# Performance work log

Measured on AMD Instinct MI355X. Metric: run time of the kernel, lower is better.

## Reference

```python
import jax, jax.numpy as jnp
import numpy as np

B, R, C, H, W, N = 8, 50, 150, 128, 128, 4096
K = 192  # >= ceil(diagonal of 128x128) = 180, padded line-sample budget
LOSS_WEIGHT = 0.1


def setup_inputs() -> dict:
    key = jax.random.key(0)
    ks = jax.random.split(key, 8)
    rafs = jax.random.normal(ks[0], (B, 2 * R, H, W), jnp.float32)
    heatmaps = jax.random.uniform(ks[1], (B, C, H, W), jnp.float32, minval=0.05, maxval=1.0)
    bi = jax.random.randint(ks[2], (N,), 0, B)
    scls = jax.random.randint(ks[3], (N,), 0, C)
    ocls = jax.random.randint(ks[4], (N,), 0, C)
    syx = jax.random.randint(ks[5], (N, 2), 0, H)
    oyx = jax.random.randint(ks[6], (N, 2), 0, W)
    pred = jax.random.randint(ks[7], (N,), 0, R)
    # ensure subj center != obj center so every relation has nonzero norm (valid)
    same = jnp.all(syx == oyx, axis=1)
    oyx = oyx.at[:, 1].set(jnp.where(same, (oyx[:, 1] + 1) % W, oyx[:, 1]))
    rels = jnp.concatenate(
        [bi[:, None], scls[:, None], syx, ocls[:, None], oyx, pred[:, None]], axis=1
    ).astype(jnp.int32)
    return {"rafs": rafs, "heatmaps": heatmaps, "rels": rels}


def _relation_loss(rafs, heatmaps, rels):
    b, _, h, w = rafs.shape
    raf = jnp.clip(rafs, -1.0, 1.0).reshape(b, -1, 2, h, w)  # [B, R, 2, H, W]
    bi, scls, sy, sx, ocls, oy, ox, pred = (rels[:, i] for i in range(8))
    subj_s = heatmaps[bi, scls, sy, sx]  # [N]
    obj_s = heatmaps[bi, ocls, oy, ox]   # [N]
    # relation unit vector in (x, y) order, obj - subj
    dx = (ox - sx).astype(jnp.float32)
    dy = (oy - sy).astype(jnp.float32)
    norms = jnp.sqrt(dx * dx + dy * dy)  # > 0 by construction (all valid)
    ux, uy = dx / norms, dy / norms
    num = jnp.ceil(norms).astype(jnp.int32)  # number of linspace samples per relation
    # linspace from obj -> subj (matches np.linspace(obj, subj, num)) padded to K
    t = jnp.arange(K, dtype=jnp.float32)[None, :] / jnp.maximum(num - 1, 1).astype(jnp.float32)[:, None]
    px = jnp.rint(ox.astype(jnp.float32)[:, None] + t * (sx - ox).astype(jnp.float32)[:, None]).astype(jnp.int32)
    py = jnp.rint(oy.astype(jnp.float32)[:, None] + t * (sy - oy).astype(jnp.float32)[:, None]).astype(jnp.int32)
    in_len = jnp.arange(K)[None, :] < num[:, None]
    # np.unique dedup: rounded points along a monotone segment repeat only consecutively
    dup = jnp.concatenate(
        [jnp.zeros((px.shape[0], 1), bool), (px[:, 1:] == px[:, :-1]) & (py[:, 1:] == py[:, :-1])],
        axis=1,
    )
    valid = in_len & ~dup  # [N, K]
    vals = raf[bi[:, None], pred[:, None], :, py, px]  # [N, K, 2] gather along the line
    dots = vals[..., 0] * ux[:, None] + vals[..., 1] * uy[:, None]  # [N, K]
    cnt = valid.sum(axis=1).astype(jnp.float32)
    integral = jnp.where(valid, dots, 0.0).sum(axis=1) / cnt  # mean over unique line points
    rel_scores = subj_s * obj_s * jnp.clip(integral, 0.0, 1.0)
    # BCE vs target=1: -log(p) (torch clamps log at -100; eps keeps grads finite)
    logp = jnp.log(jnp.maximum(rel_scores, 1e-12))
    return -logp.mean() * LOSS_WEIGHT


def reference(rafs, heatmaps, rels):
    return _relation_loss(rafs, heatmaps, rels)
```

## Files before the change

kernel.cpp:

```cpp
#include <hip/hip_runtime.h>
#include <math.h>

#define KPTS   192
#define RDIM   50
#define HDIM   128
#define WDIM   128
#define NREL   4096
#define CDIM   150
#define LOSS_W 0.1f
#define WPB    4
#define BLK    (WPB * 64)
#define PLANE  (HDIM * WDIM)

__global__ __launch_bounds__(BLK) void relation_partial_kernel(
    const float* __restrict__ rafs,
    const float* __restrict__ heatmaps,
    const int*   __restrict__ rels,
    float* __restrict__ ws)
{
    const int wave = threadIdx.x >> 6;
    const int lane = threadIdx.x & 63;
    const int rel  = blockIdx.x * WPB + wave;

    const int4* r4 = (const int4*)(rels + (size_t)rel * 8);
    const int4 ra = r4[0];
    const int4 rb = r4[1];
    const int bi   = __builtin_amdgcn_readfirstlane(ra.x);
    const int scls = __builtin_amdgcn_readfirstlane(ra.y);
    const int sy   = __builtin_amdgcn_readfirstlane(ra.z);
    const int sx   = __builtin_amdgcn_readfirstlane(ra.w);
    const int ocls = __builtin_amdgcn_readfirstlane(rb.x);
    const int oy   = __builtin_amdgcn_readfirstlane(rb.y);
    const int ox   = __builtin_amdgcn_readfirstlane(rb.z);
    const int pred = __builtin_amdgcn_readfirstlane(rb.w);

    const float subj = heatmaps[(((size_t)bi * CDIM + (size_t)scls) * HDIM + (size_t)sy) * WDIM + (size_t)sx];
    const float obj  = heatmaps[(((size_t)bi * CDIM + (size_t)ocls) * HDIM + (size_t)oy) * WDIM + (size_t)ox];

    const float dx = (float)(ox - sx);
    const float dy = (float)(oy - sy);
    const float norms = sqrtf(dx * dx + dy * dy);
    const float ux = dx / norms;
    const float uy = dy / norms;
    const int   num = (int)ceilf(norms);
    const float denom = (float)((num - 1) > 1 ? (num - 1) : 1);

    const float oxf = (float)ox, oyf = (float)oy;
    const float sxmox = (float)(sx - ox);
    const float symoy = (float)(sy - oy);

    const size_t rafbase =
        ((size_t)bi * (2 * RDIM) + (size_t)(2 * pred)) * (size_t)PLANE;

    int   pxs[3], pys[3];
    float vxs[3], vys[3];

    #pragma unroll
    for (int s = 0; s < 3; ++s) {
        const int k  = lane + 64 * s;
        const int kk = (k < num) ? k : (num - 1);
        const float t  = (float)kk / denom;
        const int   px = (int)rintf(oxf + t * sxmox);
        const int   py = (int)rintf(oyf + t * symoy);
        pxs[s] = px;
        pys[s] = py;
        const size_t off = (size_t)py * WDIM + (size_t)px;
        vxs[s] = rafs[rafbase + off];
        vys[s] = rafs[rafbase + (size_t)PLANE + off];
    }

    float dot  = 0.0f;
    int   vcnt = 0;
    int   px63 = -1, py63 = -1;

    #pragma unroll
    for (int s = 0; s < 3; ++s) {
        int pxp = __shfl_up(pxs[s], 1, 64);
        int pyp = __shfl_up(pys[s], 1, 64);
        if (lane == 0) { pxp = px63; pyp = py63; }
        px63 = __shfl(pxs[s], 63, 64);
        py63 = __shfl(pys[s], 63, 64);

        const int  k   = lane + 64 * s;
        const bool dup = (pxs[s] == pxp) && (pys[s] == pyp);
        if ((k < num) && !dup) {
            float vx = fminf(fmaxf(vxs[s], -1.0f), 1.0f);
            float vy = fminf(fmaxf(vys[s], -1.0f), 1.0f);
            dot  += vx * ux + vy * uy;
            vcnt += 1;
        }
    }

    #pragma unroll
    for (int off = 32; off > 0; off >>= 1) {
        dot  += __shfl_down(dot,  off, 64);
        vcnt += __shfl_down(vcnt, off, 64);
    }

    if (lane == 0) {
        float integral = dot / (float)vcnt;
        integral = fminf(fmaxf(integral, 0.0f), 1.0f);
        const float rs = subj * obj * integral;
        ws[rel] = logf(fmaxf(rs, 1e-12f));
    }
}

__global__ __launch_bounds__(256) void reduce_kernel(
    const float* __restrict__ part,
    float* __restrict__ out)
{
    const int tid = threadIdx.x;
    float acc = 0.0f;
    #pragma unroll
    for (int j = 0; j < NREL / 256; ++j)
        acc += part[tid + j * 256];

    #pragma unroll
    for (int off = 32; off > 0; off >>= 1)
        acc += __shfl_down(acc, off, 64);

    __shared__ float s[4];
    const int wave = tid >> 6;
    const int lane = tid & 63;
    if (lane == 0) s[wave] = acc;
    __syncthreads();
    if (tid == 0) {
        const float total = s[0] + s[1] + s[2] + s[3];
        out[0] = total * (-LOSS_W / (float)NREL);
    }
}

extern "C" void kernel_launch(void* const* d_in, const int* in_sizes, int n_in,
                              void* d_out, int out_size, void* d_ws, size_t ws_size,
                              hipStream_t stream) {
    const float* rafs     = (const float*)d_in[0];
    const float* heatmaps = (const float*)d_in[1];
    const int*   rels     = (const int*)d_in[2];
    float*       out      = (float*)d_out;
    float*       part     = (float*)d_ws;

    relation_partial_kernel<<<NREL / WPB, BLK, 0, stream>>>(rafs, heatmaps, rels, part);
    reduce_kernel<<<1, 256, 0, stream>>>(part, out);
}
```

Baseline: 138.7 us.

## Stage each RAF plane pair in LDS and bucket relations per block

```diff
diff --git a/kernel.cpp b/kernel.cpp
--- a/kernel.cpp
+++ b/kernel.cpp
@@ -3,105 +3,135 @@
 
 #define KPTS   192
 #define RDIM   50
+#define BDIM   8
 #define HDIM   128
 #define WDIM   128
 #define NREL   4096
 #define CDIM   150
 #define LOSS_W 0.1f
 #define WPB    4
-#define BLK    (WPB * 64)
 #define PLANE  (HDIM * WDIM)
+#define NPAIR  (BDIM * RDIM)
+#define LISTSZ 512
 
-__global__ __launch_bounds__(BLK) void relation_partial_kernel(
+__global__ __launch_bounds__(256) void relation_lds_kernel(
     const float* __restrict__ rafs,
     const float* __restrict__ heatmaps,
     const int*   __restrict__ rels,
     float* __restrict__ ws)
 {
-    const int wave = threadIdx.x >> 6;
-    const int lane = threadIdx.x & 63;
-    const int rel  = blockIdx.x * WPB + wave;
+    __shared__ float plane[2 * PLANE];
+    __shared__ int   list[LISTSZ];
+    __shared__ int   lcnt;
 
-    const int4* r4 = (const int4*)(rels + (size_t)rel * 8);
-    const int4 ra = r4[0];
-    const int4 rb = r4[1];
-    const int bi   = __builtin_amdgcn_readfirstlane(ra.x);
-    const int scls = __builtin_amdgcn_readfirstlane(ra.y);
-    const int sy   = __builtin_amdgcn_readfirstlane(ra.z);
-    const int sx   = __builtin_amdgcn_readfirstlane(ra.w);
-    const int ocls = __builtin_amdgcn_readfirstlane(rb.x);
-    const int oy   = __builtin_amdgcn_readfirstlane(rb.y);
-    const int ox   = __builtin_amdgcn_readfirstlane(rb.z);
-    const int pred = __builtin_amdgcn_readfirstlane(rb.w);
+    const int tid  = threadIdx.x;
+    const int bi_b = blockIdx.x / RDIM;
+    const int pr_b = blockIdx.x - bi_b * RDIM;
 
-    const float subj = heatmaps[(((size_t)bi * CDIM + (size_t)scls) * HDIM + (size_t)sy) * WDIM + (size_t)sx];
-    const float obj  = heatmaps[(((size_t)bi * CDIM + (size_t)ocls) * HDIM + (size_t)oy) * WDIM + (size_t)ox];
+    if (tid == 0) lcnt = 0;
+    __syncthreads();
 
-    const float dx = (float)(ox - sx);
-    const float dy = (float)(oy - sy);
-    const float norms = sqrtf(dx * dx + dy * dy);
-    const float ux = dx / norms;
-    const float uy = dy / norms;
-    const int   num = (int)ceilf(norms);
-    const float denom = (float)((num - 1) > 1 ? (num - 1) : 1);
-
-    const float oxf = (float)ox, oyf = (float)oy;
-    const float sxmox = (float)(sx - ox);
-    const float symoy = (float)(sy - oy);
-
-    const size_t rafbase =
-        ((size_t)bi * (2 * RDIM) + (size_t)(2 * pred)) * (size_t)PLANE;
-
-    int   pxs[3], pys[3];
-    float vxs[3], vys[3];
-
-    #pragma unroll
-    for (int s = 0; s < 3; ++s) {
-        const int k  = lane + 64 * s;
-        const int kk = (k < num) ? k : (num - 1);
-        const float t  = (float)kk / denom;
-        const int   px = (int)rintf(oxf + t * sxmox);
-        const int   py = (int)rintf(oyf + t * symoy);
-        pxs[s] = px;
-        pys[s] = py;
-        const size_t off = (size_t)py * WDIM + (size_t)px;
-        vxs[s] = rafs[rafbase + off];
-        vys[s] = rafs[rafbase + (size_t)PLANE + off];
-    }
-
-    float dot  = 0.0f;
-    int   vcnt = 0;
-    int   px63 = -1, py63 = -1;
-
-    #pragma unroll
-    for (int s = 0; s < 3; ++s) {
-        int pxp = __shfl_up(pxs[s], 1, 64);
-        int pyp = __shfl_up(pys[s], 1, 64);
-        if (lane == 0) { pxp = px63; pyp = py63; }
-        px63 = __shfl(pxs[s], 63, 64);
-        py63 = __shfl(pys[s], 63, 64);
-
-        const int  k   = lane + 64 * s;
-        const bool dup = (pxs[s] == pxp) && (pys[s] == pyp);
-        if ((k < num) && !dup) {
-            float vx = fminf(fmaxf(vxs[s], -1.0f), 1.0f);
-            float vy = fminf(fmaxf(vys[s], -1.0f), 1.0f);
-            dot  += vx * ux + vy * uy;
-            vcnt += 1;
+    for (int i = tid; i < NREL; i += 256) {
+        const int rbi = rels[i * 8 + 0];
+        const int rpr = rels[i * 8 + 7];
+        if (rbi == bi_b && rpr == pr_b) {
+            const int p = atomicAdd(&lcnt, 1);
+            if (p < LISTSZ) list[p] = i;
         }
     }
 
-    #pragma unroll
-    for (int off = 32; off > 0; off >>= 1) {
-        dot  += __shfl_down(dot,  off, 64);
-        vcnt += __shfl_down(vcnt, off, 64);
+    {
+        const size_t rafbase =
+            ((size_t)bi_b * (2 * RDIM) + (size_t)(2 * pr_b)) * (size_t)PLANE;
+        const float4* __restrict__ src = (const float4*)(rafs + rafbase);
+        float4* dst = (float4*)plane;
+        #pragma unroll 8
+        for (int i = tid; i < (2 * PLANE) / 4; i += 256)
+            dst[i] = src[i];
     }
+    __syncthreads();
 
-    if (lane == 0) {
-        float integral = dot / (float)vcnt;
-        integral = fminf(fmaxf(integral, 0.0f), 1.0f);
-        const float rs = subj * obj * integral;
-        ws[rel] = logf(fmaxf(rs, 1e-12f));
+    const int n    = lcnt;
+    const int wave = tid >> 6;
+    const int lane = tid & 63;
+
+    for (int j = wave; j < n; j += WPB) {
+        const int rel = __builtin_amdgcn_readfirstlane(list[j]);
+
+        const int4* r4 = (const int4*)(rels + (size_t)rel * 8);
+        const int4 ra = r4[0];
+        const int4 rb = r4[1];
+        const int scls = __builtin_amdgcn_readfirstlane(ra.y);
+        const int sy   = __builtin_amdgcn_readfirstlane(ra.z);
+        const int sx   = __builtin_amdgcn_readfirstlane(ra.w);
+        const int ocls = __builtin_amdgcn_readfirstlane(rb.x);
+        const int oy   = __builtin_amdgcn_readfirstlane(rb.y);
+        const int ox   = __builtin_amdgcn_readfirstlane(rb.z);
+
+        const float subj = heatmaps[(((size_t)bi_b * CDIM + (size_t)scls) * HDIM + (size_t)sy) * WDIM + (size_t)sx];
+        const float obj  = heatmaps[(((size_t)bi_b * CDIM + (size_t)ocls) * HDIM + (size_t)oy) * WDIM + (size_t)ox];
+
+        const float dx = (float)(ox - sx);
+        const float dy = (float)(oy - sy);
+        const float norms = sqrtf(dx * dx + dy * dy);
+        const float ux = dx / norms;
+        const float uy = dy / norms;
+        const int   num = (int)ceilf(norms);
+        const float denom = (float)((num - 1) > 1 ? (num - 1) : 1);
+
+        const float oxf = (float)ox, oyf = (float)oy;
+        const float sxmox = (float)(sx - ox);
+        const float symoy = (float)(sy - oy);
+
+        int   pxs[3], pys[3];
+        float vxs[3], vys[3];
+        #pragma unroll
+        for (int s = 0; s < 3; ++s) {
+            const int k  = lane + 64 * s;
+            const int kk = (k < num) ? k : (num - 1);
+            const float t  = (float)kk / denom;
+            const int   px = (int)rintf(oxf + t * sxmox);
+            const int   py = (int)rintf(oyf + t * symoy);
+            pxs[s] = px;
+            pys[s] = py;
+            const int off = py * WDIM + px;
+            vxs[s] = plane[off];
+            vys[s] = plane[PLANE + off];
+        }
+
+        float dot  = 0.0f;
+        int   vcnt = 0;
+        int   px63 = -1, py63 = -1;
+        #pragma unroll
+        for (int s = 0; s < 3; ++s) {
+            int pxp = __shfl_up(pxs[s], 1, 64);
+            int pyp = __shfl_up(pys[s], 1, 64);
+            if (lane == 0) { pxp = px63; pyp = py63; }
+            px63 = __shfl(pxs[s], 63, 64);
+            py63 = __shfl(pys[s], 63, 64);
+
+            const int  k   = lane + 64 * s;
+            const bool dup = (pxs[s] == pxp) && (pys[s] == pyp);
+            if ((k < num) && !dup) {
+                float vx = fminf(fmaxf(vxs[s], -1.0f), 1.0f);
+                float vy = fminf(fmaxf(vys[s], -1.0f), 1.0f);
+                dot  += vx * ux + vy * uy;
+                vcnt += 1;
+            }
+        }
+
+        #pragma unroll
+        for (int off = 32; off > 0; off >>= 1) {
+            dot  += __shfl_down(dot,  off, 64);
+            vcnt += __shfl_down(vcnt, off, 64);
+        }
+
+        if (lane == 0) {
+            float integral = dot / (float)vcnt;
+            integral = fminf(fmaxf(integral, 0.0f), 1.0f);
+            const float rs = subj * obj * integral;
+            ws[rel] = logf(fmaxf(rs, 1e-12f));
+        }
     }
 }
 
@@ -139,6 +169,6 @@
     float*       out      = (float*)d_out;
     float*       part     = (float*)d_ws;
 
-    relation_partial_kernel<<<NREL / WPB, BLK, 0, stream>>>(rafs, heatmaps, rels, part);
+    relation_lds_kernel<<<NPAIR, 256, 0, stream>>>(rafs, heatmaps, rels, part);
     reduce_kernel<<<1, 256, 0, stream>>>(part, out);
 }
```

Measured after the change: 161.3 us. +16.3%, slower.

## Fuse final reduction via last-block atomic and stream-warm raf tensor into cache

Applied to the files above, without the earlier changes.

```diff
diff --git a/kernel.cpp b/kernel.cpp
--- a/kernel.cpp
+++ b/kernel.cpp
@@ -3,6 +3,7 @@
 
 #define KPTS   192
 #define RDIM   50
+#define BDIM   8
 #define HDIM   128
 #define WDIM   128
 #define NREL   4096
@@ -11,15 +12,20 @@
 #define WPB    4
 #define BLK    (WPB * 64)
 #define PLANE  (HDIM * WDIM)
+#define NBLOCKS (NREL / WPB)
+#define RAF_F4  (BDIM * 2 * RDIM * PLANE / 4)
+#define PF_PER_BLOCK (RAF_F4 / NBLOCKS)
 
-__global__ __launch_bounds__(BLK) void relation_partial_kernel(
+__global__ __launch_bounds__(BLK) void relation_fused_kernel(
     const float* __restrict__ rafs,
     const float* __restrict__ heatmaps,
     const int*   __restrict__ rels,
-    float* __restrict__ ws)
+    float* __restrict__ ws,
+    float* __restrict__ out)
 {
-    const int wave = threadIdx.x >> 6;
-    const int lane = threadIdx.x & 63;
+    const int tid  = threadIdx.x;
+    const int wave = tid >> 6;
+    const int lane = tid & 63;
     const int rel  = blockIdx.x * WPB + wave;
 
     const int4* r4 = (const int4*)(rels + (size_t)rel * 8);
@@ -52,9 +58,19 @@
     const size_t rafbase =
         ((size_t)bi * (2 * RDIM) + (size_t)(2 * pred)) * (size_t)PLANE;
 
+    {
+        const float4* __restrict__ src = (const float4*)rafs;
+        const int base = blockIdx.x * PF_PER_BLOCK;
+        float kx = 0.f, ky = 0.f, kz = 0.f, kw = 0.f;
+        for (int i = tid; i < PF_PER_BLOCK; i += BLK) {
+            const float4 v = src[base + i];
+            kx += v.x; ky += v.y; kz += v.z; kw += v.w;
+        }
+        asm volatile("" :: "v"(kx), "v"(ky), "v"(kz), "v"(kw));
+    }
+
     int   pxs[3], pys[3];
     float vxs[3], vys[3];
-
     #pragma unroll
     for (int s = 0; s < 3; ++s) {
         const int k  = lane + 64 * s;
@@ -72,7 +88,6 @@
     float dot  = 0.0f;
     int   vcnt = 0;
     int   px63 = -1, py63 = -1;
-
     #pragma unroll
     for (int s = 0; s < 3; ++s) {
         int pxp = __shfl_up(pxs[s], 1, 64);
@@ -103,30 +118,35 @@
         const float rs = subj * obj * integral;
         ws[rel] = logf(fmaxf(rs, 1e-12f));
     }
-}
 
-__global__ __launch_bounds__(256) void reduce_kernel(
-    const float* __restrict__ part,
-    float* __restrict__ out)
-{
-    const int tid = threadIdx.x;
-    float acc = 0.0f;
-    #pragma unroll
-    for (int j = 0; j < NREL / 256; ++j)
-        acc += part[tid + j * 256];
-
-    #pragma unroll
-    for (int off = 32; off > 0; off >>= 1)
-        acc += __shfl_down(acc, off, 64);
-
-    __shared__ float s[4];
-    const int wave = tid >> 6;
-    const int lane = tid & 63;
-    if (lane == 0) s[wave] = acc;
+    __shared__ int amLast;
     __syncthreads();
     if (tid == 0) {
-        const float total = s[0] + s[1] + s[2] + s[3];
-        out[0] = total * (-LOSS_W / (float)NREL);
+        __threadfence();
+        int* cnt = (int*)(ws + NREL);
+        const int old = atomicAdd(cnt, 1);
+        amLast = (old == NBLOCKS - 1) ? 1 : 0;
+        if (amLast) __threadfence();
+    }
+    __syncthreads();
+
+    if (amLast) {
+        float acc = 0.0f;
+        #pragma unroll
+        for (int j = 0; j < NREL / BLK; ++j)
+            acc += ws[tid + j * BLK];
+
+        #pragma unroll
+        for (int off = 32; off > 0; off >>= 1)
+            acc += __shfl_down(acc, off, 64);
+
+        __shared__ float s[WPB];
+        if (lane == 0) s[wave] = acc;
+        __syncthreads();
+        if (tid == 0) {
+            const float total = s[0] + s[1] + s[2] + s[3];
+            out[0] = total * (-LOSS_W / (float)NREL);
+        }
     }
 }
 
@@ -139,6 +159,7 @@
     float*       out      = (float*)d_out;
     float*       part     = (float*)d_ws;
 
-    relation_partial_kernel<<<NREL / WPB, BLK, 0, stream>>>(rafs, heatmaps, rels, part);
-    reduce_kernel<<<1, 256, 0, stream>>>(part, out);
+    hipMemsetAsync((void*)(part + NREL), 0, sizeof(int), stream);
+
+    relation_fused_kernel<<<NBLOCKS, BLK, 0, stream>>>(rafs, heatmaps, rels, part, out);
 }
```

Measured after the change: 174.8 us. 1.26x slower.
